# Optimization experiments

Hardware: AMD Instinct MI355X
Metric: run time of the kernel (lower is better)

The kernel has to match this reference:

```python
import jax, jax.numpy as jnp
import numpy as np

REFINE_CONF = 0.968  # cfg['refine_conf']


def setup_inputs() -> dict:
    key = jax.random.key(0)
    ks = jax.random.split(key, 6)
    return {
        "source_queue": jax.random.normal(ks[0], (512, 512, 16, 16), jnp.float32),
        "tgt_feat": jax.random.normal(ks[1], (2, 512, 16, 16), jnp.float32),
        "tgt_logits": jax.random.normal(ks[2], (2, 19, 256, 256), jnp.float32),
        "auged_feat": jax.random.normal(ks[3], (2, 16, 512, 16, 16), jnp.float32),
        "auged_logits": jax.random.normal(ks[4], (2, 16, 19, 256, 256), jnp.float32),
        "pseudo_label": jax.random.randint(ks[5], (2, 256, 256), 0, 19, jnp.int32),
        "k": 5,
    }


def reference(source_queue, tgt_feat, tgt_logits, auged_feat, auged_logits, pseudo_label, k):
    Q = source_queue.shape[0]
    queue_flat = source_queue.reshape(Q, -1)          # [Q, D], D = 512*16*16
    B = tgt_feat.shape[0]
    tgt_flat = tgt_feat.reshape(B, -1)                # [B, D]
    A = auged_feat.shape[1]
    auged_flat = auged_feat.reshape(B, A, -1)         # [B, A, D]
    auged_soft = jax.nn.softmax(auged_logits, axis=2)  # softmax over classes: [B, A, C, H, W]

    def per_sample(t_flat, a_flat, a_soft):
        # cdist of one target feature against the whole queue
        dist = jnp.linalg.norm(queue_flat - t_flat[None, :], axis=1)   # [Q]
        i_min = jnp.argmin(dist)
        closest_feature = queue_flat[i_min]                             # [D]
        closest_distance = dist[i_min]                                  # scalar
        # distances of augmented features to the closest source feature
        d2 = jnp.linalg.norm(a_flat - closest_feature[None, :], axis=1)  # [A]
        mask = d2 <= closest_distance
        masked = jnp.where(mask, d2, jnp.inf)
        # k smallest masked distances (inf entries = filtered out)
        neg_vals, idx = jax.lax.top_k(-masked, k)                       # [k]
        w = jnp.isfinite(neg_vals).astype(a_soft.dtype)                 # valid = within mask count
        sel = a_soft[idx]                                               # [k, C, H, W]
        avg = jnp.einsum('kchw,k->chw', sel, w) / jnp.maximum(w.sum(), 1.0)
        return avg, mask.sum()

    avg_soft, counts = jax.vmap(per_sample)(tgt_flat, auged_flat, auged_soft)  # [B,C,H,W], [B]
    knn_labels = jnp.argmax(avg_soft, axis=1).astype(pseudo_label.dtype)       # [B,H,W]
    # if no augmented feature passed the threshold, fall back to original pseudo label
    labels = jnp.where((counts > 0)[:, None, None], knn_labels, pseudo_label)
    # only refine low-confidence pixels
    tgt_soft = jax.nn.softmax(tgt_logits, axis=1)
    pseudo_mask = jnp.max(tgt_soft, axis=1) < REFINE_CONF               # [B,H,W]
    refined = jnp.where(pseudo_mask, labels, pseudo_label)
    return refined, avg_soft
```

## Files before the change

kernel.cpp:

```cpp
#include <hip/hip_runtime.h>
#include <math.h>

#define D 131072
#define Q 512
#define BB 2
#define AA 16
#define CC 19
#define HW 65536
#define REFINE_CONF 0.968f

#define CH1 4
#define CH2 8

__global__ __launch_bounds__(256) void k_dist2(const float* __restrict__ queue,
                                               const float* __restrict__ tgt,
                                               float* __restrict__ part) {
    const int q  = blockIdx.x;
    const int ch = blockIdx.y;
    const int t  = threadIdx.x;
    const int off4 = ch * (D / CH1 / 4);
    const float4* __restrict__ qr = (const float4*)(queue + (size_t)q * D) + off4;
    const float4* __restrict__ t0 = (const float4*)(tgt) + off4;
    const float4* __restrict__ t1 = (const float4*)(tgt + D) + off4;
    float a0 = 0.f, a1 = 0.f;
#pragma unroll 4
    for (int i = t; i < D / CH1 / 4; i += 256) {
        float4 qv = qr[i];
        float4 u  = t0[i];
        float4 v  = t1[i];
        float d;
        d = qv.x - u.x; a0 = fmaf(d, d, a0);
        d = qv.y - u.y; a0 = fmaf(d, d, a0);
        d = qv.z - u.z; a0 = fmaf(d, d, a0);
        d = qv.w - u.w; a0 = fmaf(d, d, a0);
        d = qv.x - v.x; a1 = fmaf(d, d, a1);
        d = qv.y - v.y; a1 = fmaf(d, d, a1);
        d = qv.z - v.z; a1 = fmaf(d, d, a1);
        d = qv.w - v.w; a1 = fmaf(d, d, a1);
    }
    for (int o = 32; o > 0; o >>= 1) { a0 += __shfl_down(a0, o); a1 += __shfl_down(a1, o); }
    __shared__ float s0[4], s1[4];
    int lane = t & 63, wid = t >> 6;
    if (lane == 0) { s0[wid] = a0; s1[wid] = a1; }
    __syncthreads();
    if (t == 0) {
        part[(size_t)q * CH1 + ch]            = s0[0] + s0[1] + s0[2] + s0[3];
        part[(size_t)(Q + q) * CH1 + ch]      = s1[0] + s1[1] + s1[2] + s1[3];
    }
}

__global__ __launch_bounds__(512) void k_argmin(const float* __restrict__ part,
                                                int* __restrict__ imin,
                                                float* __restrict__ minval) {
    const int b = blockIdx.x;
    const int t = threadIdx.x;
    __shared__ float sv[512];
    __shared__ int   si[512];
    const float* p = part + (size_t)(b * Q + t) * CH1;
    sv[t] = p[0] + p[1] + p[2] + p[3];
    si[t] = t;
    __syncthreads();
    for (int s = 256; s > 0; s >>= 1) {
        if (t < s) {
            float v2 = sv[t + s]; int i2 = si[t + s];
            if (v2 < sv[t] || (v2 == sv[t] && i2 < si[t])) { sv[t] = v2; si[t] = i2; }
        }
        __syncthreads();
    }
    if (t == 0) { imin[b] = si[0]; minval[b] = sv[0]; }
}

__global__ __launch_bounds__(256) void k_d2(const float* __restrict__ queue,
                                            const float* __restrict__ auged,
                                            const int* __restrict__ imin,
                                            float* __restrict__ part2) {
    const int ba = blockIdx.x;
    const int ch = blockIdx.y;
    const int b  = ba >> 4;
    const int t  = threadIdx.x;
    const int off4 = ch * (D / CH2 / 4);
    const float4* __restrict__ cr = (const float4*)(queue + (size_t)imin[b] * D) + off4;
    const float4* __restrict__ ar = (const float4*)(auged + (size_t)ba * D) + off4;
    float acc = 0.f;
#pragma unroll 4
    for (int i = t; i < D / CH2 / 4; i += 256) {
        float4 c4 = cr[i];
        float4 a4 = ar[i];
        float d;
        d = a4.x - c4.x; acc = fmaf(d, d, acc);
        d = a4.y - c4.y; acc = fmaf(d, d, acc);
        d = a4.z - c4.z; acc = fmaf(d, d, acc);
        d = a4.w - c4.w; acc = fmaf(d, d, acc);
    }
    for (int o = 32; o > 0; o >>= 1) acc += __shfl_down(acc, o);
    __shared__ float s0[4];
    int lane = t & 63, wid = t >> 6;
    if (lane == 0) s0[wid] = acc;
    __syncthreads();
    if (t == 0) part2[(size_t)ba * CH2 + ch] = s0[0] + s0[1] + s0[2] + s0[3];
}

__global__ __launch_bounds__(64) void k_select(const float* __restrict__ part2,
                                               const float* __restrict__ minval,
                                               const int* __restrict__ kptr,
                                               int* __restrict__ selidx,
                                               float* __restrict__ wsel,
                                               float* __restrict__ wsumdiv,
                                               int* __restrict__ countspos) {
    __shared__ float s_d2[BB * AA];
    const int t = threadIdx.x;
    if (t < BB * AA) {
        const float* p = part2 + (size_t)t * CH2;
        float s = 0.f;
#pragma unroll
        for (int c = 0; c < CH2; ++c) s += p[c];
        s_d2[t] = s;
    }
    __syncthreads();
    const int b = t;
    if (b >= BB) return;
    int k = *kptr;
    if (k > AA) k = AA;
    if (k < 0) k = 0;
    const float cd = sqrtf(minval[b]);
    float vals[AA];
    int cnt = 0;
    for (int a = 0; a < AA; ++a) {
        float dd = sqrtf(s_d2[b * AA + a]);
        bool m = (dd <= cd);
        if (m) cnt++;
        vals[a] = m ? dd : INFINITY;
    }
    float ws = 0.f;
    for (int kk = 0; kk < k; ++kk) {
        int bi = 0; float bv = vals[0];
        for (int a = 1; a < AA; ++a)
            if (vals[a] < bv) { bv = vals[a]; bi = a; }
        selidx[b * AA + kk] = bi;
        float w = isinf(bv) ? 0.f : 1.f;
        wsel[b * AA + kk] = w;
        ws += w;
        vals[bi] = INFINITY;
    }
    for (int kk = k; kk < AA; ++kk) { selidx[b * AA + kk] = 0; wsel[b * AA + kk] = 0.f; }
    wsumdiv[b]   = fmaxf(ws, 1.f);
    countspos[b] = (cnt > 0) ? 1 : 0;
}

__global__ __launch_bounds__(256) void k_refine(const float* __restrict__ auged_logits,
                                                const float* __restrict__ tgt_logits,
                                                const int*   __restrict__ pseudo,
                                                const int*   __restrict__ selidx,
                                                const float* __restrict__ wsel,
                                                const float* __restrict__ wsumdiv,
                                                const int*   __restrict__ countspos,
                                                const int*   __restrict__ kptr,
                                                float* __restrict__ out_refined,
                                                float* __restrict__ out_avg) {
    const int p = blockIdx.x * 256 + threadIdx.x;
    const int b   = p >> 16;
    const int pix = p & (HW - 1);

    __shared__ int   s_idx[AA];
    __shared__ float s_w[AA];
    __shared__ float s_wd;
    __shared__ int   s_cp;
    __shared__ int   s_k;
    if (threadIdx.x == 0) {
        s_wd = wsumdiv[b];
        s_cp = countspos[b];
        int k = *kptr; if (k > AA) k = AA; if (k < 0) k = 0;
        s_k = k;
    }
    if (threadIdx.x < AA) {
        s_idx[threadIdx.x] = selidx[b * AA + threadIdx.x];
        s_w[threadIdx.x]   = wsel[b * AA + threadIdx.x];
    }
    __syncthreads();

    float acc[CC];
#pragma unroll
    for (int c = 0; c < CC; ++c) acc[c] = 0.f;

    const int k = s_k;
    for (int kk = 0; kk < k; ++kk) {
        if (s_w[kk] == 0.f) break;
        const int a = s_idx[kk];
        const float* base = auged_logits + ((size_t)(b * AA + a) * CC) * HW + pix;
        float l[CC];
        float m = -INFINITY;
#pragma unroll
        for (int c = 0; c < CC; ++c) { l[c] = base[(size_t)c * HW]; m = fmaxf(m, l[c]); }
        float se = 0.f;
#pragma unroll
        for (int c = 0; c < CC; ++c) { l[c] = expf(l[c] - m); se += l[c]; }
        float rse = 1.f / se;
#pragma unroll
        for (int c = 0; c < CC; ++c) acc[c] = fmaf(l[c], rse, acc[c]);
    }

    const float wd = s_wd;
    int best = 0; float bv = -INFINITY;
#pragma unroll
    for (int c = 0; c < CC; ++c) {
        float av = acc[c] / wd;
        out_avg[((size_t)(b * CC + c)) * HW + pix] = av;
        if (av > bv) { bv = av; best = c; }
    }

    const float* tb = tgt_logits + (size_t)b * CC * HW + pix;
    float tl[CC];
    float tm = -INFINITY;
#pragma unroll
    for (int c = 0; c < CC; ++c) { tl[c] = tb[(size_t)c * HW]; tm = fmaxf(tm, tl[c]); }
    float tse = 0.f;
#pragma unroll
    for (int c = 0; c < CC; ++c) tse += expf(tl[c] - tm);
    const float pmax = 1.f / tse;

    const int pl      = pseudo[p];
    const int label   = s_cp ? best : pl;
    const int refined = (pmax < REFINE_CONF) ? label : pl;
    out_refined[p] = (float)refined;
}

extern "C" void kernel_launch(void* const* d_in, const int* in_sizes, int n_in,
                              void* d_out, int out_size, void* d_ws, size_t ws_size,
                              hipStream_t stream) {
    const float* queue        = (const float*)d_in[0];
    const float* tgt          = (const float*)d_in[1];
    const float* tgt_logits   = (const float*)d_in[2];
    const float* auged_feat   = (const float*)d_in[3];
    const float* auged_logits = (const float*)d_in[4];
    const int*   pseudo       = (const int*)d_in[5];
    const int*   kptr         = (const int*)d_in[6];

    float* ws        = (float*)d_ws;
    float* part      = ws;
    float* part2     = ws + 4096;
    float* minval    = ws + 4352;
    int*   imin      = (int*)(ws + 4354);
    int*   selidx    = (int*)(ws + 4356);
    float* wsel      = ws + 4388;
    float* wsumdiv   = ws + 4420;
    int*   countspos = (int*)(ws + 4422);

    float* out_refined = (float*)d_out;
    float* out_avg     = (float*)d_out + BB * HW;

    hipLaunchKernelGGL(k_dist2,  dim3(Q, CH1),       dim3(256), 0, stream, queue, tgt, part);
    hipLaunchKernelGGL(k_argmin, dim3(BB),           dim3(512), 0, stream, part, imin, minval);
    hipLaunchKernelGGL(k_d2,     dim3(BB * AA, CH2), dim3(256), 0, stream, queue, auged_feat, imin, part2);
    hipLaunchKernelGGL(k_select, dim3(1),            dim3(64),  0, stream, part2, minval, kptr,
                       selidx, wsel, wsumdiv, countspos);
    hipLaunchKernelGGL(k_refine, dim3((BB * HW) / 256), dim3(256), 0, stream,
                       auged_logits, tgt_logits, pseudo, selidx, wsel, wsumdiv, countspos, kptr,
                       out_refined, out_avg);
}
```

Measured before the change: 462.7 us.

## Fold argmin and top-k selection into consumer kernels, prefetch next logits

Removes the separate argmin and selection kernels. Each block of the distance-to-augmented kernel and each block of the refine kernel now recomputes the argmin over the 512 partial sums itself, and thread 0 of every refine block redoes the k-nearest selection. This saves two launches and their serialization gaps. In exchange, every one of the 512 refine blocks does redundant shared-memory reductions and a serial selection before it can start. The refine loop also loads target logits early and prefetches the next selected sample's logits while the current one is processed, which raises register pressure.

```diff
diff --git a/kernel.cpp b/kernel.cpp
--- a/kernel.cpp
+++ b/kernel.cpp
@@ -44,42 +44,44 @@
     if (lane == 0) { s0[wid] = a0; s1[wid] = a1; }
     __syncthreads();
     if (t == 0) {
-        part[(size_t)q * CH1 + ch]            = s0[0] + s0[1] + s0[2] + s0[3];
-        part[(size_t)(Q + q) * CH1 + ch]      = s1[0] + s1[1] + s1[2] + s1[3];
-    }
-}
-
-__global__ __launch_bounds__(512) void k_argmin(const float* __restrict__ part,
-                                                int* __restrict__ imin,
-                                                float* __restrict__ minval) {
-    const int b = blockIdx.x;
-    const int t = threadIdx.x;
-    __shared__ float sv[512];
-    __shared__ int   si[512];
-    const float* p = part + (size_t)(b * Q + t) * CH1;
-    sv[t] = p[0] + p[1] + p[2] + p[3];
-    si[t] = t;
-    __syncthreads();
-    for (int s = 256; s > 0; s >>= 1) {
+        part[(size_t)q * CH1 + ch]       = s0[0] + s0[1] + s0[2] + s0[3];
+        part[(size_t)(Q + q) * CH1 + ch] = s1[0] + s1[1] + s1[2] + s1[3];
+    }
+}
+
+__device__ __forceinline__ void fold_argmin(const float* __restrict__ part, int b, int t,
+                                            float* sv, int* si) {
+    const float* p0 = part + (size_t)(b * Q + t) * CH1;
+    const float* p1 = part + (size_t)(b * Q + t + 256) * CH1;
+    float v0 = p0[0] + p0[1] + p0[2] + p0[3];
+    float v1 = p1[0] + p1[1] + p1[2] + p1[3];
+    if (v1 < v0) { sv[t] = v1; si[t] = t + 256; }
+    else         { sv[t] = v0; si[t] = t; }
+    __syncthreads();
+    for (int s = 128; s > 0; s >>= 1) {
         if (t < s) {
             float v2 = sv[t + s]; int i2 = si[t + s];
             if (v2 < sv[t] || (v2 == sv[t] && i2 < si[t])) { sv[t] = v2; si[t] = i2; }
         }
         __syncthreads();
     }
-    if (t == 0) { imin[b] = si[0]; minval[b] = sv[0]; }
 }
 
 __global__ __launch_bounds__(256) void k_d2(const float* __restrict__ queue,
                                             const float* __restrict__ auged,
-                                            const int* __restrict__ imin,
+                                            const float* __restrict__ part,
                                             float* __restrict__ part2) {
     const int ba = blockIdx.x;
     const int ch = blockIdx.y;
     const int b  = ba >> 4;
     const int t  = threadIdx.x;
+    __shared__ float sv[256];
+    __shared__ int   si[256];
+    fold_argmin(part, b, t, sv, si);
+    const int im = si[0];
+
     const int off4 = ch * (D / CH2 / 4);
-    const float4* __restrict__ cr = (const float4*)(queue + (size_t)imin[b] * D) + off4;
+    const float4* __restrict__ cr = (const float4*)(queue + (size_t)im * D) + off4;
     const float4* __restrict__ ar = (const float4*)(auged + (size_t)ba * D) + off4;
     float acc = 0.f;
 #pragma unroll 4
@@ -100,103 +102,101 @@
     if (t == 0) part2[(size_t)ba * CH2 + ch] = s0[0] + s0[1] + s0[2] + s0[3];
 }
 
-__global__ __launch_bounds__(64) void k_select(const float* __restrict__ part2,
-                                               const float* __restrict__ minval,
-                                               const int* __restrict__ kptr,
-                                               int* __restrict__ selidx,
-                                               float* __restrict__ wsel,
-                                               float* __restrict__ wsumdiv,
-                                               int* __restrict__ countspos) {
-    __shared__ float s_d2[BB * AA];
-    const int t = threadIdx.x;
-    if (t < BB * AA) {
-        const float* p = part2 + (size_t)t * CH2;
-        float s = 0.f;
-#pragma unroll
-        for (int c = 0; c < CH2; ++c) s += p[c];
-        s_d2[t] = s;
-    }
-    __syncthreads();
-    const int b = t;
-    if (b >= BB) return;
-    int k = *kptr;
-    if (k > AA) k = AA;
-    if (k < 0) k = 0;
-    const float cd = sqrtf(minval[b]);
-    float vals[AA];
-    int cnt = 0;
-    for (int a = 0; a < AA; ++a) {
-        float dd = sqrtf(s_d2[b * AA + a]);
-        bool m = (dd <= cd);
-        if (m) cnt++;
-        vals[a] = m ? dd : INFINITY;
-    }
-    float ws = 0.f;
-    for (int kk = 0; kk < k; ++kk) {
-        int bi = 0; float bv = vals[0];
-        for (int a = 1; a < AA; ++a)
-            if (vals[a] < bv) { bv = vals[a]; bi = a; }
-        selidx[b * AA + kk] = bi;
-        float w = isinf(bv) ? 0.f : 1.f;
-        wsel[b * AA + kk] = w;
-        ws += w;
-        vals[bi] = INFINITY;
-    }
-    for (int kk = k; kk < AA; ++kk) { selidx[b * AA + kk] = 0; wsel[b * AA + kk] = 0.f; }
-    wsumdiv[b]   = fmaxf(ws, 1.f);
-    countspos[b] = (cnt > 0) ? 1 : 0;
-}
-
 __global__ __launch_bounds__(256) void k_refine(const float* __restrict__ auged_logits,
                                                 const float* __restrict__ tgt_logits,
                                                 const int*   __restrict__ pseudo,
-                                                const int*   __restrict__ selidx,
-                                                const float* __restrict__ wsel,
-                                                const float* __restrict__ wsumdiv,
-                                                const int*   __restrict__ countspos,
+                                                const float* __restrict__ part,
+                                                const float* __restrict__ part2,
                                                 const int*   __restrict__ kptr,
                                                 float* __restrict__ out_refined,
                                                 float* __restrict__ out_avg) {
-    const int p = blockIdx.x * 256 + threadIdx.x;
+    const int p   = blockIdx.x * 256 + threadIdx.x;
     const int b   = p >> 16;
     const int pix = p & (HW - 1);
+    const int t   = threadIdx.x;
+
+    __shared__ float sv[256];
+    __shared__ int   si[256];
+    fold_argmin(part, b, t, sv, si);
+    __shared__ float s_d2[AA];
+    if (t < AA) {
+        const float* pp = part2 + (size_t)(b * AA + t) * CH2;
+        float s = 0.f;
+#pragma unroll
+        for (int c = 0; c < CH2; ++c) s += pp[c];
+        s_d2[t] = s;
+    }
+    __syncthreads();
 
     __shared__ int   s_idx[AA];
-    __shared__ float s_w[AA];
+    __shared__ int   s_kv;
+    __shared__ int   s_cp;
     __shared__ float s_wd;
-    __shared__ int   s_cp;
-    __shared__ int   s_k;
-    if (threadIdx.x == 0) {
-        s_wd = wsumdiv[b];
-        s_cp = countspos[b];
+    if (t == 0) {
         int k = *kptr; if (k > AA) k = AA; if (k < 0) k = 0;
-        s_k = k;
-    }
-    if (threadIdx.x < AA) {
-        s_idx[threadIdx.x] = selidx[b * AA + threadIdx.x];
-        s_w[threadIdx.x]   = wsel[b * AA + threadIdx.x];
-    }
-    __syncthreads();
+        const float cd = sqrtf(sv[0]);
+        float vals[AA];
+        int cnt = 0;
+        for (int a = 0; a < AA; ++a) {
+            float dd = sqrtf(s_d2[a]);
+            bool m = (dd <= cd);
+            if (m) cnt++;
+            vals[a] = m ? dd : INFINITY;
+        }
+        int kv = 0;
+        for (int kk = 0; kk < k; ++kk) {
+            int bi = 0; float bv = vals[0];
+            for (int a = 1; a < AA; ++a)
+                if (vals[a] < bv) { bv = vals[a]; bi = a; }
+            s_idx[kk] = bi;
+            if (!isinf(bv)) kv++;
+            vals[bi] = INFINITY;
+        }
+        s_kv = kv;
+        s_wd = fmaxf((float)kv, 1.f);
+        s_cp = (cnt > 0) ? 1 : 0;
+    }
+    __syncthreads();
+
+    const int kv = s_kv;
+    const int pl = pseudo[p];
+
+    const float* tb = tgt_logits + (size_t)b * CC * HW + pix;
+    float tl[CC];
+#pragma unroll
+    for (int c = 0; c < CC; ++c) tl[c] = tb[(size_t)c * HW];
 
     float acc[CC];
 #pragma unroll
     for (int c = 0; c < CC; ++c) acc[c] = 0.f;
 
-    const int k = s_k;
-    for (int kk = 0; kk < k; ++kk) {
-        if (s_w[kk] == 0.f) break;
-        const int a = s_idx[kk];
-        const float* base = auged_logits + ((size_t)(b * AA + a) * CC) * HW + pix;
-        float l[CC];
+    float lc[CC];
+    if (kv > 0) {
+        const float* base = auged_logits + ((size_t)(b * AA + s_idx[0]) * CC) * HW + pix;
+#pragma unroll
+        for (int c = 0; c < CC; ++c) lc[c] = base[(size_t)c * HW];
+    }
+    for (int kk = 0; kk < kv; ++kk) {
+        float ln[CC];
+        const bool more = (kk + 1 < kv);
+        if (more) {
+            const float* base = auged_logits + ((size_t)(b * AA + s_idx[kk + 1]) * CC) * HW + pix;
+#pragma unroll
+            for (int c = 0; c < CC; ++c) ln[c] = base[(size_t)c * HW];
+        }
         float m = -INFINITY;
 #pragma unroll
-        for (int c = 0; c < CC; ++c) { l[c] = base[(size_t)c * HW]; m = fmaxf(m, l[c]); }
+        for (int c = 0; c < CC; ++c) m = fmaxf(m, lc[c]);
         float se = 0.f;
 #pragma unroll
-        for (int c = 0; c < CC; ++c) { l[c] = expf(l[c] - m); se += l[c]; }
+        for (int c = 0; c < CC; ++c) { lc[c] = expf(lc[c] - m); se += lc[c]; }
         float rse = 1.f / se;
 #pragma unroll
-        for (int c = 0; c < CC; ++c) acc[c] = fmaf(l[c], rse, acc[c]);
+        for (int c = 0; c < CC; ++c) acc[c] = fmaf(lc[c], rse, acc[c]);
+        if (more) {
+#pragma unroll
+            for (int c = 0; c < CC; ++c) lc[c] = ln[c];
+        }
     }
 
     const float wd = s_wd;
@@ -208,17 +208,14 @@
         if (av > bv) { bv = av; best = c; }
     }
 
-    const float* tb = tgt_logits + (size_t)b * CC * HW + pix;
-    float tl[CC];
     float tm = -INFINITY;
 #pragma unroll
-    for (int c = 0; c < CC; ++c) { tl[c] = tb[(size_t)c * HW]; tm = fmaxf(tm, tl[c]); }
+    for (int c = 0; c < CC; ++c) tm = fmaxf(tm, tl[c]);
     float tse = 0.f;
 #pragma unroll
     for (int c = 0; c < CC; ++c) tse += expf(tl[c] - tm);
     const float pmax = 1.f / tse;
 
-    const int pl      = pseudo[p];
     const int label   = s_cp ? best : pl;
     const int refined = (pmax < REFINE_CONF) ? label : pl;
     out_refined[p] = (float)refined;
@@ -235,25 +232,16 @@
     const int*   pseudo       = (const int*)d_in[5];
     const int*   kptr         = (const int*)d_in[6];
 
-    float* ws        = (float*)d_ws;
-    float* part      = ws;
-    float* part2     = ws + 4096;
-    float* minval    = ws + 4352;
-    int*   imin      = (int*)(ws + 4354);
-    int*   selidx    = (int*)(ws + 4356);
-    float* wsel      = ws + 4388;
-    float* wsumdiv   = ws + 4420;
-    int*   countspos = (int*)(ws + 4422);
+    float* ws    = (float*)d_ws;
+    float* part  = ws;
+    float* part2 = ws + 4096;
 
     float* out_refined = (float*)d_out;
     float* out_avg     = (float*)d_out + BB * HW;
 
-    hipLaunchKernelGGL(k_dist2,  dim3(Q, CH1),       dim3(256), 0, stream, queue, tgt, part);
-    hipLaunchKernelGGL(k_argmin, dim3(BB),           dim3(512), 0, stream, part, imin, minval);
-    hipLaunchKernelGGL(k_d2,     dim3(BB * AA, CH2), dim3(256), 0, stream, queue, auged_feat, imin, part2);
-    hipLaunchKernelGGL(k_select, dim3(1),            dim3(64),  0, stream, part2, minval, kptr,
-                       selidx, wsel, wsumdiv, countspos);
+    hipLaunchKernelGGL(k_dist2, dim3(Q, CH1),       dim3(256), 0, stream, queue, tgt, part);
+    hipLaunchKernelGGL(k_d2,    dim3(BB * AA, CH2), dim3(256), 0, stream, queue, auged_feat, part, part2);
     hipLaunchKernelGGL(k_refine, dim3((BB * HW) / 256), dim3(256), 0, stream,
-                       auged_logits, tgt_logits, pseudo, selidx, wsel, wsumdiv, countspos, kptr,
+                       auged_logits, tgt_logits, pseudo, part, part2, kptr,
                        out_refined, out_avg);
 }
```

Result: no change. 461.6 us (-0.2%).
